# Kernel tuning notes

Measured on AMD Instinct MI355X. Metric: run time of the kernel, lower is better.

## Reference

```python
import jax, jax.numpy as jnp
import numpy as np

N_HEAD = 4

def setup_inputs() -> dict:
    key = jax.random.key(0)
    ks = jax.random.split(key, 10)
    B, N, C = 4, 16384, 256
    s = 1.0 / np.sqrt(C)
    inp = {
        'x': jax.random.normal(ks[0], (B, N, C), dtype=jnp.float32),
        'mask_x': jnp.ones((B, N), dtype=jnp.float32),
        'mask_y': jnp.ones((B, N), dtype=jnp.float32),
        'Wq': jax.random.normal(ks[1], (C, C), dtype=jnp.float32) * s,
        'bq': jnp.zeros((C,), dtype=jnp.float32),
        'Wk': jax.random.normal(ks[2], (C, C), dtype=jnp.float32) * s,
        'bk': jnp.zeros((C,), dtype=jnp.float32),
        'Wv': jax.random.normal(ks[3], (C, C), dtype=jnp.float32) * s,
        'bv': jnp.zeros((C,), dtype=jnp.float32),
        'Wp': jax.random.normal(ks[4], (C, C), dtype=jnp.float32) * s,
        'bp': jnp.zeros((C,), dtype=jnp.float32),
    }
    return inp

def reference(x, mask_x, mask_y, Wq, bq, Wk, bk, Wv, bv, Wp, bp):
    B, N, C = x.shape
    H = N_HEAD
    D = C // H
    # projections (y = x, self-attention path); weights stored [in, out]
    def split_heads(t):  # [B,N,C] -> [B,H,N,D]
        return t.reshape(B, N, H, D).transpose(0, 2, 1, 3)
    Q = split_heads(x @ Wq + bq)
    K = split_heads(x @ Wk + bk)
    V = split_heads(x @ Wv + bv)
    mx = mask_x[:, None, :, None]  # [B,1,N,1]
    my = mask_y[:, None, :, None]  # [B,1,M,1]
    K = K * my
    V = V * my
    # torch F.gelu default is exact (erf) gelu
    Q = jax.nn.gelu(Q, approximate=False) + 1.0
    K = jax.nn.gelu(K, approximate=False) + 1.0
    KV = jnp.einsum('bhmd,bhme->bhde', K, V)          # [B,H,D,D]
    K_sum = K.sum(axis=2, keepdims=True)               # [B,H,1,D]
    denom = jnp.sum(Q * K_sum, axis=-1, keepdims=True) # [B,H,N,1]
    attn_out = jnp.einsum('bhnd,bhde->bhne', Q, KV) / denom
    attn_out = attn_out * mx
    out = attn_out.transpose(0, 2, 1, 3).reshape(B, N, C)
    return out @ Wp + bp
```

## Files before the change

kernel.cpp:

```cpp
#include <hip/hip_runtime.h>
#include <hip/hip_bf16.h>
#include <cstdint>
#include <cstddef>

#define SEQ   16384
#define CHN   256

typedef __attribute__((ext_vector_type(8))) short  short8;
typedef __attribute__((ext_vector_type(4))) float  f32x4;

static __device__ __forceinline__ unsigned short f2bf(float f) {
    unsigned int u = __builtin_bit_cast(unsigned int, f);
    u += 0x7fffu + ((u >> 16) & 1u);
    return (unsigned short)(u >> 16);
}
static __device__ __forceinline__ float bf2f(unsigned short h) {
    unsigned int u = ((unsigned int)h) << 16;
    return __builtin_bit_cast(float, u);
}
static __device__ __forceinline__ float gelu_exact(float x) {
    return 0.5f * x * (1.0f + erff(x * 0.70710678118654752f));
}
static __device__ __forceinline__ int swz_us(int row, int kbyte) {
    return (row * 128 + (kbyte ^ ((row & 7) << 4))) >> 1;
}

__global__ __launch_bounds__(256) void prep_kernel(
    const float* __restrict__ Wq, const float* __restrict__ Wk,
    const float* __restrict__ Wv, const float* __restrict__ Wp,
    unsigned short* __restrict__ Wqt, unsigned short* __restrict__ Wkt,
    unsigned short* __restrict__ Wvt, unsigned short* __restrict__ Wpt,
    float* __restrict__ KV, float* __restrict__ Ksum)
{
    const int idx = blockIdx.x * 256 + threadIdx.x;
    const int n = idx >> 8, k = idx & 255;
    const int src = k * 256 + n;
    Wqt[idx] = f2bf(Wq[src]);
    Wkt[idx] = f2bf(Wk[src]);
    Wvt[idx] = f2bf(Wv[src]);
    Wpt[idx] = f2bf(Wp[src]);
    KV[idx] = 0.0f;
    if (idx < 1024) Ksum[idx] = 0.0f;
}

__global__ __launch_bounds__(256) void qkv_gemm(
    const float* __restrict__ x, const float* __restrict__ my,
    const unsigned short* __restrict__ Wqt, const unsigned short* __restrict__ Wkt,
    const unsigned short* __restrict__ Wvt,
    const float* __restrict__ bq, const float* __restrict__ bk,
    const float* __restrict__ bv,
    unsigned short* __restrict__ Qb, unsigned short* __restrict__ Kb,
    unsigned short* __restrict__ Vb)
{
    __shared__ unsigned short As[128 * 64];
    __shared__ unsigned short Bs[128 * 64];
    const int t = threadIdx.x;
    const int mat  = blockIdx.x >> 1;
    const int col0 = (blockIdx.x & 1) * 128;
    const long row0 = (long)blockIdx.y * 128;
    const unsigned short* Wt = (mat == 0) ? Wqt : (mat == 1) ? Wkt : Wvt;
    const float* bias        = (mat == 0) ? bq  : (mat == 1) ? bk  : bv;

    const int lane = t & 63, wave = t >> 6;
    const int wm = wave >> 1, wn = wave & 1;

    f32x4 acc[4][4];
    #pragma unroll
    for (int i = 0; i < 4; ++i)
        #pragma unroll
        for (int j = 0; j < 4; ++j) acc[i][j] = (f32x4)0.0f;

    for (int k0 = 0; k0 < 256; k0 += 64) {
        #pragma unroll
        for (int it = 0; it < 8; ++it) {
            const int idx = it * 256 + t;
            const int r = idx >> 4, c4 = (idx & 15) * 4;
            const float4 v = *(const float4*)(x + (row0 + r) * 256 + k0 + c4);
            uint2 pk;
            pk.x = (unsigned int)f2bf(v.x) | ((unsigned int)f2bf(v.y) << 16);
            pk.y = (unsigned int)f2bf(v.z) | ((unsigned int)f2bf(v.w) << 16);
            *(uint2*)&As[swz_us(r, c4 * 2)] = pk;
        }
        #pragma unroll
        for (int it = 0; it < 4; ++it) {
            const int idx = it * 256 + t;
            const int n = idx >> 3, c8 = (idx & 7) * 8;
            const uint4 v = *(const uint4*)(Wt + (size_t)(col0 + n) * 256 + k0 + c8);
            *(uint4*)&Bs[swz_us(n, c8 * 2)] = v;
        }
        __syncthreads();
        #pragma unroll
        for (int kk = 0; kk < 2; ++kk) {
            const int kbyte = kk * 64 + (lane >> 4) * 16;
            short8 af[4], bfr[4];
            #pragma unroll
            for (int mi = 0; mi < 4; ++mi) {
                const int r = wm * 64 + mi * 16 + (lane & 15);
                af[mi] = *(const short8*)&As[swz_us(r, kbyte)];
            }
            #pragma unroll
            for (int ni = 0; ni < 4; ++ni) {
                const int n = wn * 64 + ni * 16 + (lane & 15);
                bfr[ni] = *(const short8*)&Bs[swz_us(n, kbyte)];
            }
            #pragma unroll
            for (int mi = 0; mi < 4; ++mi)
                #pragma unroll
                for (int ni = 0; ni < 4; ++ni)
                    acc[mi][ni] = __builtin_amdgcn_mfma_f32_16x16x32_bf16(
                        af[mi], bfr[ni], acc[mi][ni], 0, 0, 0);
        }
        __syncthreads();
    }
    unsigned short* Ob = (mat == 0) ? Qb : (mat == 1) ? Kb : Vb;
    #pragma unroll
    for (int ni = 0; ni < 4; ++ni) {
        const int coll = col0 + wn * 64 + ni * 16 + (lane & 15);
        const float bc = bias[coll];
        #pragma unroll
        for (int mi = 0; mi < 4; ++mi) {
            const int lr0 = wm * 64 + mi * 16 + ((lane >> 4) << 2);
            #pragma unroll
            for (int r = 0; r < 4; ++r) {
                const long grow = row0 + lr0 + r;
                float val = acc[mi][ni][r] + bc;
                if (mat == 0)      val = gelu_exact(val) + 1.0f;
                else if (mat == 1) val = gelu_exact(val * my[grow]) + 1.0f;
                else               val = val * my[grow];
                Ob[grow * 256 + coll] = f2bf(val);
            }
        }
    }
}

__global__ __launch_bounds__(256) void kv_reduce(
    const unsigned short* __restrict__ Kb, const unsigned short* __restrict__ Vb,
    float* __restrict__ KV, float* __restrict__ Ksum)
{
    __shared__ float kf[16][64];
    __shared__ float vf[16][64];
    const int t = threadIdx.x;
    const int bh = blockIdx.y;
    const long base = (long)(bh >> 2) * SEQ * 256 + (bh & 3) * 64;
    const long m0 = (long)blockIdx.x * 1024;
    const int d0 = (t >> 4) * 4, e0 = (t & 15) * 4;
    const int sr = t >> 4, swhich = (t >> 3) & 1, sseg = t & 7;
    float acc[4][4] = {};
    float ks[4] = {};
    for (int it = 0; it < 64; ++it) {
        const long row = m0 + it * 16 + sr;
        const unsigned short* src = (swhich ? Vb : Kb) + base + row * 256 + sseg * 8;
        const uint4 raw = *(const uint4*)src;
        const unsigned short* rh = (const unsigned short*)&raw;
        float* dst = swhich ? &vf[sr][sseg * 8] : &kf[sr][sseg * 8];
        #pragma unroll
        for (int j = 0; j < 8; ++j) dst[j] = bf2f(rh[j]);
        __syncthreads();
        #pragma unroll
        for (int mm = 0; mm < 16; ++mm) {
            const float4 kd = *(const float4*)&kf[mm][d0];
            const float4 ve = *(const float4*)&vf[mm][e0];
            const float k4[4] = {kd.x, kd.y, kd.z, kd.w};
            const float v4[4] = {ve.x, ve.y, ve.z, ve.w};
            #pragma unroll
            for (int i = 0; i < 4; ++i)
                #pragma unroll
                for (int j = 0; j < 4; ++j) acc[i][j] += k4[i] * v4[j];
            if ((t & 15) == 0) {
                #pragma unroll
                for (int i = 0; i < 4; ++i) ks[i] += k4[i];
            }
        }
        __syncthreads();
    }
    #pragma unroll
    for (int i = 0; i < 4; ++i)
        #pragma unroll
        for (int j = 0; j < 4; ++j)
            atomicAdd(&KV[((size_t)bh * 64 + d0 + i) * 64 + e0 + j], acc[i][j]);
    if ((t & 15) == 0) {
        #pragma unroll
        for (int i = 0; i < 4; ++i) atomicAdd(&Ksum[bh * 64 + d0 + i], ks[i]);
    }
}

__global__ __launch_bounds__(256) void attn_kernel(
    const unsigned short* __restrict__ Qb, const float* __restrict__ KV,
    const float* __restrict__ Ksum, const float* __restrict__ mx,
    unsigned short* __restrict__ Ab)
{
    __shared__ unsigned short Qs[128 * 64];
    __shared__ unsigned short KVT[64 * 64];
    __shared__ float ksh[64];
    __shared__ float sden[128];
    const int t = threadIdx.x;
    const long row0 = (long)blockIdx.x * 128;
    const int b = (int)(row0 >> 14);
    const int lane = t & 63, wave = t >> 6, wm = wave >> 1, wn = wave & 1;

    for (int h = 0; h < 4; ++h) {
        const int bh = b * 4 + h;
        #pragma unroll
        for (int it = 0; it < 4; ++it) {
            const int idx = it * 256 + t;
            const int r = idx >> 3, c8 = (idx & 7) * 8;
            const uint4 v = *(const uint4*)(Qb + (row0 + r) * 256 + h * 64 + c8);
            *(uint4*)&Qs[swz_us(r, c8 * 2)] = v;
        }
        {
            const int e = t & 63, dg = t >> 6;
            #pragma unroll
            for (int i = 0; i < 16; ++i) {
                const int d = dg * 16 + i;
                const float v = KV[((size_t)bh * 64 + d) * 64 + e];
                KVT[(e * 128 + ((d * 2) ^ ((e & 7) << 4))) >> 1] = f2bf(v);
            }
        }
        if (t < 64) ksh[t] = Ksum[bh * 64 + t];
        __syncthreads();
        if (t < 128) {
            float s = 0.0f;
            for (int d = 0; d < 64; ++d)
                s += bf2f(Qs[swz_us(t, d * 2)]) * ksh[d];
            sden[t] = mx[row0 + t] / s;
        }
        __syncthreads();
        f32x4 acc[4][2];
        #pragma unroll
        for (int i = 0; i < 4; ++i) { acc[i][0] = (f32x4)0.0f; acc[i][1] = (f32x4)0.0f; }
        #pragma unroll
        for (int kk = 0; kk < 2; ++kk) {
            const int kbyte = kk * 64 + (lane >> 4) * 16;
            short8 af[4], bfr[2];
            #pragma unroll
            for (int mi = 0; mi < 4; ++mi) {
                const int r = wm * 64 + mi * 16 + (lane & 15);
                af[mi] = *(const short8*)&Qs[swz_us(r, kbyte)];
            }
            #pragma unroll
            for (int ni = 0; ni < 2; ++ni) {
                const int e = wn * 32 + ni * 16 + (lane & 15);
                bfr[ni] = *(const short8*)&KVT[swz_us(e, kbyte)];
            }
            #pragma unroll
            for (int mi = 0; mi < 4; ++mi)
                #pragma unroll
                for (int ni = 0; ni < 2; ++ni)
                    acc[mi][ni] = __builtin_amdgcn_mfma_f32_16x16x32_bf16(
                        af[mi], bfr[ni], acc[mi][ni], 0, 0, 0);
        }
        #pragma unroll
        for (int ni = 0; ni < 2; ++ni) {
            const int e = wn * 32 + ni * 16 + (lane & 15);
            #pragma unroll
            for (int mi = 0; mi < 4; ++mi) {
                const int lr0 = wm * 64 + mi * 16 + ((lane >> 4) << 2);
                #pragma unroll
                for (int r = 0; r < 4; ++r) {
                    const int lr = lr0 + r;
                    const float val = acc[mi][ni][r] * sden[lr];
                    Ab[(row0 + lr) * 256 + h * 64 + e] = f2bf(val);
                }
            }
        }
        __syncthreads();
    }
}

__global__ __launch_bounds__(256) void proj_gemm(
    const unsigned short* __restrict__ Ab, const unsigned short* __restrict__ Wpt,
    const float* __restrict__ bp, float* __restrict__ out)
{
    __shared__ unsigned short As[128 * 64];
    __shared__ unsigned short Bs[128 * 64];
    const int t = threadIdx.x;
    const int col0 = blockIdx.x * 128;
    const long row0 = (long)blockIdx.y * 128;
    const int lane = t & 63, wave = t >> 6, wm = wave >> 1, wn = wave & 1;

    f32x4 acc[4][4];
    #pragma unroll
    for (int i = 0; i < 4; ++i)
        #pragma unroll
        for (int j = 0; j < 4; ++j) acc[i][j] = (f32x4)0.0f;

    for (int k0 = 0; k0 < 256; k0 += 64) {
        #pragma unroll
        for (int it = 0; it < 4; ++it) {
            const int idx = it * 256 + t;
            const int r = idx >> 3, c8 = (idx & 7) * 8;
            const uint4 v = *(const uint4*)(Ab + (row0 + r) * 256 + k0 + c8);
            *(uint4*)&As[swz_us(r, c8 * 2)] = v;
        }
        #pragma unroll
        for (int it = 0; it < 4; ++it) {
            const int idx = it * 256 + t;
            const int n = idx >> 3, c8 = (idx & 7) * 8;
            const uint4 v = *(const uint4*)(Wpt + (size_t)(col0 + n) * 256 + k0 + c8);
            *(uint4*)&Bs[swz_us(n, c8 * 2)] = v;
        }
        __syncthreads();
        #pragma unroll
        for (int kk = 0; kk < 2; ++kk) {
            const int kbyte = kk * 64 + (lane >> 4) * 16;
            short8 af[4], bfr[4];
            #pragma unroll
            for (int mi = 0; mi < 4; ++mi) {
                const int r = wm * 64 + mi * 16 + (lane & 15);
                af[mi] = *(const short8*)&As[swz_us(r, kbyte)];
            }
            #pragma unroll
            for (int ni = 0; ni < 4; ++ni) {
                const int n = wn * 64 + ni * 16 + (lane & 15);
                bfr[ni] = *(const short8*)&Bs[swz_us(n, kbyte)];
            }
            #pragma unroll
            for (int mi = 0; mi < 4; ++mi)
                #pragma unroll
                for (int ni = 0; ni < 4; ++ni)
                    acc[mi][ni] = __builtin_amdgcn_mfma_f32_16x16x32_bf16(
                        af[mi], bfr[ni], acc[mi][ni], 0, 0, 0);
        }
        __syncthreads();
    }
    #pragma unroll
    for (int ni = 0; ni < 4; ++ni) {
        const int coll = col0 + wn * 64 + ni * 16 + (lane & 15);
        const float bc = bp[coll];
        #pragma unroll
        for (int mi = 0; mi < 4; ++mi) {
            const int lr0 = wm * 64 + mi * 16 + ((lane >> 4) << 2);
            #pragma unroll
            for (int r = 0; r < 4; ++r) {
                const long grow = row0 + lr0 + r;
                out[grow * 256 + coll] = acc[mi][ni][r] + bc;
            }
        }
    }
}

extern "C" void kernel_launch(void* const* d_in, const int* in_sizes, int n_in,
                              void* d_out, int out_size, void* d_ws, size_t ws_size,
                              hipStream_t stream)
{
    (void)in_sizes; (void)n_in; (void)out_size; (void)ws_size;
    const float* x  = (const float*)d_in[0];
    const float* mx = (const float*)d_in[1];
    const float* my = (const float*)d_in[2];
    const float* Wq = (const float*)d_in[3];
    const float* bq = (const float*)d_in[4];
    const float* Wk = (const float*)d_in[5];
    const float* bk = (const float*)d_in[6];
    const float* Wv = (const float*)d_in[7];
    const float* bv = (const float*)d_in[8];
    const float* Wp = (const float*)d_in[9];
    const float* bp = (const float*)d_in[10];
    float* out = (float*)d_out;

    const size_t nelem = (size_t)4 * SEQ * CHN;
    char* w = (char*)d_ws;
    unsigned short* Qb  = (unsigned short*)w; w += nelem * 2;
    unsigned short* Kb  = (unsigned short*)w; w += nelem * 2;
    unsigned short* Vb  = (unsigned short*)w; w += nelem * 2;
    unsigned short* Wqt = (unsigned short*)w; w += 131072;
    unsigned short* Wkt = (unsigned short*)w; w += 131072;
    unsigned short* Wvt = (unsigned short*)w; w += 131072;
    unsigned short* Wpt = (unsigned short*)w; w += 131072;
    float* KV   = (float*)w; w += 262144;
    float* Ksum = (float*)w; w += 4096;
    unsigned short* Ab = Kb;

    prep_kernel<<<256, 256, 0, stream>>>(Wq, Wk, Wv, Wp, Wqt, Wkt, Wvt, Wpt, KV, Ksum);
    qkv_gemm<<<dim3(6, 512), 256, 0, stream>>>(x, my, Wqt, Wkt, Wvt, bq, bk, bv, Qb, Kb, Vb);
    kv_reduce<<<dim3(16, 16), 256, 0, stream>>>(Kb, Vb, KV, Ksum);
    attn_kernel<<<512, 256, 0, stream>>>(Qb, KV, Ksum, mx, Ab);
    proj_gemm<<<dim3(2, 512), 256, 0, stream>>>(Ab, Wpt, bp, out);
}
```

Measured before the change: 413.5 us.

## Stage full x row tile once in LDS and loop over all output column tiles

The QKV and projection GEMMs now load a 128-row tile of the full 256-wide input into LDS once per block, converting x to bf16 a single time. Each block then loops over all six (or two) output column tiles, reading weight fragments directly from global memory instead of staging them through LDS. This removes the repeated x reads and bf16 conversions done by each of the six column blocks. It costs 64KB of LDS per block, which lowers occupancy, and adds uncoalesced global weight loads in the inner loop. The kv_reduce grid is also widened so each block handles a quarter as many rows, giving more parallelism at the price of more atomic accumulations.

```diff
diff --git a/kernel.cpp b/kernel.cpp
--- a/kernel.cpp
+++ b/kernel.cpp
@@ -23,6 +23,9 @@
 }
 static __device__ __forceinline__ int swz_us(int row, int kbyte) {
     return (row * 128 + (kbyte ^ ((row & 7) << 4))) >> 1;
+}
+static __device__ __forceinline__ int swzA(int row, int kbyte) {
+    return (row * 512 + (kbyte ^ ((row & 7) << 4))) >> 1;
 }
 
 __global__ __launch_bounds__(256) void prep_kernel(
@@ -52,56 +55,52 @@
     unsigned short* __restrict__ Qb, unsigned short* __restrict__ Kb,
     unsigned short* __restrict__ Vb)
 {
-    __shared__ unsigned short As[128 * 64];
-    __shared__ unsigned short Bs[128 * 64];
+    __shared__ unsigned short As[128 * 256];
+    __shared__ float mys[128];
     const int t = threadIdx.x;
-    const int mat  = blockIdx.x >> 1;
-    const int col0 = (blockIdx.x & 1) * 128;
-    const long row0 = (long)blockIdx.y * 128;
-    const unsigned short* Wt = (mat == 0) ? Wqt : (mat == 1) ? Wkt : Wvt;
-    const float* bias        = (mat == 0) ? bq  : (mat == 1) ? bk  : bv;
-
-    const int lane = t & 63, wave = t >> 6;
-    const int wm = wave >> 1, wn = wave & 1;
-
-    f32x4 acc[4][4];
+    const long row0 = (long)blockIdx.x * 128;
+    const int lane = t & 63, wave = t >> 6, wm = wave >> 1, wn = wave & 1;
+
     #pragma unroll
-    for (int i = 0; i < 4; ++i)
-        #pragma unroll
-        for (int j = 0; j < 4; ++j) acc[i][j] = (f32x4)0.0f;
-
-    for (int k0 = 0; k0 < 256; k0 += 64) {
-        #pragma unroll
-        for (int it = 0; it < 8; ++it) {
-            const int idx = it * 256 + t;
-            const int r = idx >> 4, c4 = (idx & 15) * 4;
-            const float4 v = *(const float4*)(x + (row0 + r) * 256 + k0 + c4);
-            uint2 pk;
-            pk.x = (unsigned int)f2bf(v.x) | ((unsigned int)f2bf(v.y) << 16);
-            pk.y = (unsigned int)f2bf(v.z) | ((unsigned int)f2bf(v.w) << 16);
-            *(uint2*)&As[swz_us(r, c4 * 2)] = pk;
-        }
-        #pragma unroll
-        for (int it = 0; it < 4; ++it) {
-            const int idx = it * 256 + t;
-            const int n = idx >> 3, c8 = (idx & 7) * 8;
-            const uint4 v = *(const uint4*)(Wt + (size_t)(col0 + n) * 256 + k0 + c8);
-            *(uint4*)&Bs[swz_us(n, c8 * 2)] = v;
-        }
-        __syncthreads();
-        #pragma unroll
-        for (int kk = 0; kk < 2; ++kk) {
-            const int kbyte = kk * 64 + (lane >> 4) * 16;
+    for (int it = 0; it < 32; ++it) {
+        const int idx = it * 256 + t;
+        const int r = idx >> 6, c4 = (idx & 63) * 4;
+        const float4 v = *(const float4*)(x + (row0 + r) * 256 + c4);
+        uint2 pk;
+        pk.x = (unsigned int)f2bf(v.x) | ((unsigned int)f2bf(v.y) << 16);
+        pk.y = (unsigned int)f2bf(v.z) | ((unsigned int)f2bf(v.w) << 16);
+        *(uint2*)&As[swzA(r, c4 * 2)] = pk;
+    }
+    if (t < 128) mys[t] = my[row0 + t];
+    __syncthreads();
+
+    #pragma unroll 1
+    for (int ot = 0; ot < 6; ++ot) {
+        const int mat  = ot >> 1;
+        const int col0 = (ot & 1) * 128;
+        const unsigned short* Wt = (mat == 0) ? Wqt : (mat == 1) ? Wkt : Wvt;
+        const float* bias        = (mat == 0) ? bq  : (mat == 1) ? bk  : bv;
+        unsigned short* Ob       = (mat == 0) ? Qb  : (mat == 1) ? Kb  : Vb;
+
+        f32x4 acc[4][4];
+        #pragma unroll
+        for (int i = 0; i < 4; ++i)
+            #pragma unroll
+            for (int j = 0; j < 4; ++j) acc[i][j] = (f32x4)0.0f;
+
+        #pragma unroll
+        for (int kk = 0; kk < 8; ++kk) {
+            const int ke = kk * 32 + (lane >> 4) * 8;
             short8 af[4], bfr[4];
             #pragma unroll
             for (int mi = 0; mi < 4; ++mi) {
                 const int r = wm * 64 + mi * 16 + (lane & 15);
-                af[mi] = *(const short8*)&As[swz_us(r, kbyte)];
+                af[mi] = *(const short8*)&As[swzA(r, ke * 2)];
             }
             #pragma unroll
             for (int ni = 0; ni < 4; ++ni) {
-                const int n = wn * 64 + ni * 16 + (lane & 15);
-                bfr[ni] = *(const short8*)&Bs[swz_us(n, kbyte)];
+                const int n = col0 + wn * 64 + ni * 16 + (lane & 15);
+                bfr[ni] = *(const short8*)(Wt + (size_t)n * 256 + ke);
             }
             #pragma unroll
             for (int mi = 0; mi < 4; ++mi)
@@ -110,24 +109,23 @@
                     acc[mi][ni] = __builtin_amdgcn_mfma_f32_16x16x32_bf16(
                         af[mi], bfr[ni], acc[mi][ni], 0, 0, 0);
         }
-        __syncthreads();
-    }
-    unsigned short* Ob = (mat == 0) ? Qb : (mat == 1) ? Kb : Vb;
-    #pragma unroll
-    for (int ni = 0; ni < 4; ++ni) {
-        const int coll = col0 + wn * 64 + ni * 16 + (lane & 15);
-        const float bc = bias[coll];
-        #pragma unroll
-        for (int mi = 0; mi < 4; ++mi) {
-            const int lr0 = wm * 64 + mi * 16 + ((lane >> 4) << 2);
-            #pragma unroll
-            for (int r = 0; r < 4; ++r) {
-                const long grow = row0 + lr0 + r;
-                float val = acc[mi][ni][r] + bc;
-                if (mat == 0)      val = gelu_exact(val) + 1.0f;
-                else if (mat == 1) val = gelu_exact(val * my[grow]) + 1.0f;
-                else               val = val * my[grow];
-                Ob[grow * 256 + coll] = f2bf(val);
+
+        #pragma unroll
+        for (int ni = 0; ni < 4; ++ni) {
+            const int coll = col0 + wn * 64 + ni * 16 + (lane & 15);
+            const float bc = bias[coll];
+            #pragma unroll
+            for (int mi = 0; mi < 4; ++mi) {
+                const int lr0 = wm * 64 + mi * 16 + ((lane >> 4) << 2);
+                #pragma unroll
+                for (int r = 0; r < 4; ++r) {
+                    const int lr = lr0 + r;
+                    float val = acc[mi][ni][r] + bc;
+                    if (mat == 0)      val = gelu_exact(val) + 1.0f;
+                    else if (mat == 1) val = gelu_exact(val * mys[lr]) + 1.0f;
+                    else               val = val * mys[lr];
+                    Ob[(row0 + lr) * 256 + coll] = f2bf(val);
+                }
             }
         }
     }
@@ -142,12 +140,12 @@
     const int t = threadIdx.x;
     const int bh = blockIdx.y;
     const long base = (long)(bh >> 2) * SEQ * 256 + (bh & 3) * 64;
-    const long m0 = (long)blockIdx.x * 1024;
+    const long m0 = (long)blockIdx.x * 256;
     const int d0 = (t >> 4) * 4, e0 = (t & 15) * 4;
     const int sr = t >> 4, swhich = (t >> 3) & 1, sseg = t & 7;
     float acc[4][4] = {};
     float ks[4] = {};
-    for (int it = 0; it < 64; ++it) {
+    for (int it = 0; it < 16; ++it) {
         const long row = m0 + it * 16 + sr;
         const unsigned short* src = (swhich ? Vb : Kb) + base + row * 256 + sseg * 8;
         const uint4 raw = *(const uint4*)src;
@@ -271,48 +269,42 @@
     const unsigned short* __restrict__ Ab, const unsigned short* __restrict__ Wpt,
     const float* __restrict__ bp, float* __restrict__ out)
 {
-    __shared__ unsigned short As[128 * 64];
-    __shared__ unsigned short Bs[128 * 64];
+    __shared__ unsigned short As[128 * 256];
     const int t = threadIdx.x;
-    const int col0 = blockIdx.x * 128;
-    const long row0 = (long)blockIdx.y * 128;
+    const long row0 = (long)blockIdx.x * 128;
     const int lane = t & 63, wave = t >> 6, wm = wave >> 1, wn = wave & 1;
 
-    f32x4 acc[4][4];
     #pragma unroll
-    for (int i = 0; i < 4; ++i)
-        #pragma unroll
-        for (int j = 0; j < 4; ++j) acc[i][j] = (f32x4)0.0f;
-
-    for (int k0 = 0; k0 < 256; k0 += 64) {
-        #pragma unroll
-        for (int it = 0; it < 4; ++it) {
-            const int idx = it * 256 + t;
-            const int r = idx >> 3, c8 = (idx & 7) * 8;
-            const uint4 v = *(const uint4*)(Ab + (row0 + r) * 256 + k0 + c8);
-            *(uint4*)&As[swz_us(r, c8 * 2)] = v;
-        }
-        #pragma unroll
-        for (int it = 0; it < 4; ++it) {
-            const int idx = it * 256 + t;
-            const int n = idx >> 3, c8 = (idx & 7) * 8;
-            const uint4 v = *(const uint4*)(Wpt + (size_t)(col0 + n) * 256 + k0 + c8);
-            *(uint4*)&Bs[swz_us(n, c8 * 2)] = v;
-        }
-        __syncthreads();
-        #pragma unroll
-        for (int kk = 0; kk < 2; ++kk) {
-            const int kbyte = kk * 64 + (lane >> 4) * 16;
+    for (int it = 0; it < 16; ++it) {
+        const int idx = it * 256 + t;
+        const int r = idx >> 5, c8 = (idx & 31) * 8;
+        const uint4 v = *(const uint4*)(Ab + (row0 + r) * 256 + c8);
+        *(uint4*)&As[swzA(r, c8 * 2)] = v;
+    }
+    __syncthreads();
+
+    #pragma unroll 1
+    for (int ct = 0; ct < 2; ++ct) {
+        const int col0 = ct * 128;
+        f32x4 acc[4][4];
+        #pragma unroll
+        for (int i = 0; i < 4; ++i)
+            #pragma unroll
+            for (int j = 0; j < 4; ++j) acc[i][j] = (f32x4)0.0f;
+
+        #pragma unroll
+        for (int kk = 0; kk < 8; ++kk) {
+            const int ke = kk * 32 + (lane >> 4) * 8;
             short8 af[4], bfr[4];
             #pragma unroll
             for (int mi = 0; mi < 4; ++mi) {
                 const int r = wm * 64 + mi * 16 + (lane & 15);
-                af[mi] = *(const short8*)&As[swz_us(r, kbyte)];
+                af[mi] = *(const short8*)&As[swzA(r, ke * 2)];
             }
             #pragma unroll
             for (int ni = 0; ni < 4; ++ni) {
-                const int n = wn * 64 + ni * 16 + (lane & 15);
-                bfr[ni] = *(const short8*)&Bs[swz_us(n, kbyte)];
+                const int n = col0 + wn * 64 + ni * 16 + (lane & 15);
+                bfr[ni] = *(const short8*)(Wpt + (size_t)n * 256 + ke);
             }
             #pragma unroll
             for (int mi = 0; mi < 4; ++mi)
@@ -321,19 +313,19 @@
                     acc[mi][ni] = __builtin_amdgcn_mfma_f32_16x16x32_bf16(
                         af[mi], bfr[ni], acc[mi][ni], 0, 0, 0);
         }
-        __syncthreads();
-    }
-    #pragma unroll
-    for (int ni = 0; ni < 4; ++ni) {
-        const int coll = col0 + wn * 64 + ni * 16 + (lane & 15);
-        const float bc = bp[coll];
-        #pragma unroll
-        for (int mi = 0; mi < 4; ++mi) {
-            const int lr0 = wm * 64 + mi * 16 + ((lane >> 4) << 2);
-            #pragma unroll
-            for (int r = 0; r < 4; ++r) {
-                const long grow = row0 + lr0 + r;
-                out[grow * 256 + coll] = acc[mi][ni][r] + bc;
+
+        #pragma unroll
+        for (int ni = 0; ni < 4; ++ni) {
+            const int coll = col0 + wn * 64 + ni * 16 + (lane & 15);
+            const float bc = bp[coll];
+            #pragma unroll
+            for (int mi = 0; mi < 4; ++mi) {
+                const int lr0 = wm * 64 + mi * 16 + ((lane >> 4) << 2);
+                #pragma unroll
+                for (int r = 0; r < 4; ++r) {
+                    const long grow = row0 + lr0 + r;
+                    out[grow * 256 + coll] = acc[mi][ni][r] + bc;
+                }
             }
         }
     }
@@ -371,8 +363,8 @@
     unsigned short* Ab = Kb;
 
     prep_kernel<<<256, 256, 0, stream>>>(Wq, Wk, Wv, Wp, Wqt, Wkt, Wvt, Wpt, KV, Ksum);
-    qkv_gemm<<<dim3(6, 512), 256, 0, stream>>>(x, my, Wqt, Wkt, Wvt, bq, bk, bv, Qb, Kb, Vb);
-    kv_reduce<<<dim3(16, 16), 256, 0, stream>>>(Kb, Vb, KV, Ksum);
+    qkv_gemm<<<512, 256, 0, stream>>>(x, my, Wqt, Wkt, Wvt, bq, bk, bv, Qb, Kb, Vb);
+    kv_reduce<<<dim3(64, 16), 256, 0, stream>>>(Kb, Vb, KV, Ksum);
     attn_kernel<<<512, 256, 0, stream>>>(Qb, KV, Ksum, mx, Ab);
-    proj_gemm<<<dim3(2, 512), 256, 0, stream>>>(Ab, Wpt, bp, out);
-}
+    proj_gemm<<<512, 256, 0, stream>>>(Ab, Wpt, bp, out);
+}
```

New measurement: 416.4 us. About the same (+0.7%).
